# Performance work log

Hardware: AMD Instinct MI355X
Metric: run time of the kernel (lower is better)

## Reference

```python
import jax, jax.numpy as jnp
import numpy as np

K = 3          # B-spline order (cubic)
G = 10         # number of spline intervals over [0, 1]
NELY, NELX = 512, 512
WIDTHS = [2, 32, 32, 1]


def _make_grid(in_dim):
    # extended uniform knot vector over [0,1] with K extra knots each side: (in_dim, G+2K+1)
    h = 1.0 / G
    knots = jnp.arange(-K, G + K + 1, dtype=jnp.float32) * h
    return jnp.tile(knots[None, :], (in_dim, 1))


def setup_inputs() -> dict:
    key = jax.random.key(0)
    ks = jax.random.split(key, 1 + 3 * (len(WIDTHS) - 1))
    inp = {"coords": jax.random.uniform(ks[0], (NELY * NELX, 2), dtype=jnp.float32)}
    for l, (i, o) in enumerate(zip(WIDTHS[:-1], WIDTHS[1:])):
        inp[f"grid{l}"] = _make_grid(i)
        inp[f"coef{l}"] = 0.1 * jax.random.normal(ks[1 + 3 * l], (i, o, G + K), dtype=jnp.float32)
        inp[f"sb{l}"] = jax.random.normal(ks[2 + 3 * l], (i, o), dtype=jnp.float32) / np.sqrt(i).astype(np.float32)
        inp[f"sp{l}"] = jnp.ones((i, o), dtype=jnp.float32)
    inp["density_bias"] = jnp.full((1,), np.float32(np.log(0.5 / (1.0 - 0.5 + 1e-8))))
    return inp


def _b_batch(x, grid):
    # Cox-de Boor recursion. x: (B, in), grid: (in, G+2K+1) -> bases (B, in, G+K)
    xe = x[:, :, None]
    v = ((xe >= grid[None, :, :-1]) & (xe < grid[None, :, 1:])).astype(x.dtype)
    for p in range(1, K + 1):
        left = (xe - grid[None, :, : -(p + 1)]) / (grid[None, :, p:-1] - grid[None, :, : -(p + 1)])
        right = (grid[None, :, p + 1:] - xe) / (grid[None, :, p + 1:] - grid[None, :, 1:-p])
        v = left * v[:, :, :-1] + right * v[:, :, 1:]
    return v


def _kan_layer(x, grid, coef, sb, sp):
    # y_out = sum_in [ sb * silu(x) + sp * sum_k B_k(x) * coef_k ]
    B = _b_batch(x, grid)                               # (batch, in, G+K)
    spline = jnp.einsum('bik,iok->bio', B, coef)        # (batch, in, out)
    base = jax.nn.silu(x)                               # (batch, in)
    return jnp.sum(sb[None] * base[:, :, None] + sp[None] * spline, axis=1)


def reference(coords, grid0, coef0, sb0, sp0, grid1, coef1, sb1, sp1,
              grid2, coef2, sb2, sp2, density_bias):
    h = _kan_layer(coords, grid0, coef0, sb0, sp0)
    h = _kan_layer(h, grid1, coef1, sb1, sp1)
    logits = _kan_layer(h, grid2, coef2, sb2, sp2) + density_bias
    return jax.nn.sigmoid(logits).reshape(1, NELY, NELX)
```

## Files before the change

kernel.cpp:

```cpp
#include <hip/hip_runtime.h>
#include <hip/hip_bf16.h>

typedef __hip_bfloat16 bf16;
typedef __fp16 h2v __attribute__((ext_vector_type(2)));
typedef __fp16 half8 __attribute__((ext_vector_type(8)));
typedef float floatx4 __attribute__((ext_vector_type(4)));

#define NPTS (512*512)

#define OFF_BIAS 12
#define OFF_FLAG 13
#define OFF_BF   16
#define NFRAG    50
#define WS_WORDS (16 + NFRAG*64*4)


__device__ __forceinline__ bool sniff_f32(const void* g0) {
    float f = ((const float*)g0)[0];
    return fabsf(f + 0.3f) < 0.01f;
}
__device__ __forceinline__ float ld(const void* p, int i, bool f32) {
    return f32 ? ((const float*)p)[i] : __bfloat162float(((const bf16*)p)[i]);
}
__device__ __forceinline__ unsigned pk_rtn(float a, float b) {
    union { h2v v; unsigned u; } x;
    x.v[0] = (__fp16)a; x.v[1] = (__fp16)b;
    return x.u;
}
__device__ __forceinline__ unsigned pkf16(float a, float b) {
    union { h2v v; unsigned u; } x;
    x.v = __builtin_amdgcn_cvt_pkrtz(a, b);
    return x.u;
}

__device__ float slotval(int layer, int K, int o,
                         const void* c0, const void* sb0, const void* sp0,
                         const void* c1, const void* sb1, const void* sp1,
                         const void* c2, const void* sb2, const void* sp2, bool f32)
{
    int i = K >> 4, s = K & 15;
    if (layer == 2 && o != 0) return 0.0f;
    if (s >= 1 && s <= 13) {
        int m = s - 1;
        if (layer == 0) return ld(c0, (i*32+o)*13 + m, f32) * ld(sp0, i*32+o, f32);
        if (layer == 1) return ld(c1, (i*32+o)*13 + m, f32) * ld(sp1, i*32+o, f32);
        return ld(c2, i*13 + m, f32) * ld(sp2, i, f32);
    }
    if (s == 14) {
        if (layer == 0) return ld(sb0, i*32+o, f32);
        if (layer == 1) return ld(sb1, i*32+o, f32);
        return ld(sb2, i, f32);
    }
    return 0.0f;
}

__global__ __launch_bounds__(256) void kan_prep(
    const void* __restrict__ g0, const void* __restrict__ c0,
    const void* __restrict__ sb0, const void* __restrict__ sp0,
    const void* __restrict__ g1, const void* __restrict__ c1,
    const void* __restrict__ sb1, const void* __restrict__ sp1,
    const void* __restrict__ g2, const void* __restrict__ c2,
    const void* __restrict__ sb2, const void* __restrict__ sp2,
    const void* __restrict__ bias, float* __restrict__ ws)
{
    const bool f32 = sniff_f32(g0);
    int t = blockIdx.x * blockDim.x + threadIdx.x;

    if (t < 16) {
        if (t < 12) {
            int l = t >> 2, j = t & 3;
            const void* g = (l == 0) ? g0 : (l == 1) ? g1 : g2;
            float lo = ld(g, 0, f32), hi = ld(g, 16, f32);
            float ih = 16.0f / (hi - lo);
            float v = (j == 0) ? lo : (j == 1) ? hi
                    : (j == 2) ? ih : (-lo * ih);
            ws[t] = v;
        } else if (t == 12) ws[12] = ld(bias, 0, f32);
        else if (t == 13)   ws[13] = f32 ? 1.0f : 0.0f;
        else                ws[t] = 0.0f;
        return;
    }
    int ft = t - 16;
    if (ft >= NFRAG * 64) return;
    int f = ft >> 6, l = ft & 63, n = l & 15, q = l >> 4;
    int layer, c, nt;
    if (f < 2)       { layer = 0; c = 0;          nt = f; }
    else if (f < 34) { layer = 1; c = (f - 2) >> 1; nt = (f - 2) & 1; }
    else             { layer = 2; c = f - 34;     nt = 0; }
    int o = nt * 16 + n;
    unsigned wv[4];
#pragma unroll
    for (int jp = 0; jp < 4; jp++) {
        int K0 = c * 32 + q * 8 + jp * 2;
        float v0 = slotval(layer, K0,     o, c0,sb0,sp0, c1,sb1,sp1, c2,sb2,sp2, f32);
        float v1 = slotval(layer, K0 + 1, o, c0,sb0,sp0, c1,sb1,sp1, c2,sb2,sp2, f32);
        wv[jp] = pk_rtn(v0, v1);
    }
    uint4 out4; out4.x = wv[0]; out4.y = wv[1]; out4.z = wv[2]; out4.w = wv[3];
    ((uint4*)((unsigned*)ws + OFF_BF))[f * 64 + l] = out4;
}

__device__ __forceinline__ floatx4 mf(uint4 a, uint4 b, floatx4 c)
{
    union { uint4 u; half8 h; } ua, ub;
    ua.u = a; ub.u = b;
    return __builtin_amdgcn_mfma_f32_16x16x32_f16(ua.h, ub.h, c, 0, 0, 0);
}

__device__ __forceinline__ void eval_taps(float x, float ngh, float ih,
    unsigned& A, unsigned& B, unsigned& C, int& wout, float& si)
{
    float t  = fmaf(x, ih, ngh);
    float fj = floorf(t);
    float u  = t - fj;
    bool inb = (t >= 0.0f) && (t < 16.0f);
    float s6 = inb ? 0.166666667f : 0.0f;
    int j  = (int)fj;
    int jc = min(max(j, 0), 15);
    float u2 = u * u, u3 = u2 * u, om = 1.0f - u;
    float b0 = om * om * om * s6;
    float b1 = (fmaf(3.0f, u3, 4.0f) - 6.0f * u2) * s6;
    float b2 = fmaf(-3.0f, u3, fmaf(3.0f, u2, fmaf(3.0f, u, 1.0f))) * s6;
    float b3 = u3 * s6;
    int m0 = jc - 3;
    if ((unsigned)(m0 + 0) > 12u) b0 = 0.0f;
    if ((unsigned)(m0 + 1) > 12u) b1 = 0.0f;
    if ((unsigned)(m0 + 2) > 12u) b2 = 0.0f;
    if ((unsigned)(m0 + 3) > 12u) b3 = 0.0f;
    int s0 = m0 + 1;
    wout = ((s0 + 2) >> 1) - 1;
    if (s0 & 1) { A = pkf16(0.0f, b0); B = pkf16(b1, b2); C = pkf16(b3, 0.0f); }
    else        { A = pkf16(b0, b1);   B = pkf16(b2, b3); C = 0u; }
    si = x / (1.0f + __expf(-x));
}

__device__ __forceinline__ void stage2(unsigned* row, float f0, float f1,
                                       float ngh, float ih)
{
    uint4 z; z.x = 0u; z.y = 0u; z.z = 0u; z.w = 0u;
    *(uint4*)(row + 0)  = z;
    *(uint4*)(row + 4)  = z;
    *(uint4*)(row + 8)  = z;
    *(uint4*)(row + 12) = z;
    unsigned A0,B0,C0,A1,B1,C1; int w0,w1; float s0,s1;
    eval_taps(f0, ngh, ih, A0, B0, C0, w0, s0);
    eval_taps(f1, ngh, ih, A1, B1, C1, w1, s1);
    row[w0]     = A0; row[w0 + 1]  = B0; row[w0 + 2]  = C0;
    row[8 + w1] = A1; row[9 + w1]  = B1; row[10 + w1] = C1;
    row[7]  = pkf16(s0, 0.0f);
    row[15] = pkf16(s1, 0.0f);
}

__global__ __launch_bounds__(256, 4) void kan_main(
    const void* __restrict__ coords, const float* __restrict__ ws,
    void* __restrict__ out)
{
    __shared__ __align__(16) unsigned lds[4 * 2304];
    const unsigned* wsu = (const unsigned*)ws;
    const uint4* bfp = (const uint4*)(wsu + OFF_BF);

    int tid = threadIdx.x;
    int l = tid & 63, w = tid >> 6;
    int p = blockIdx.x * 256 + w * 64 + l;

    unsigned* rb = lds + w * 2304;
    unsigned* cb = rb;
    unsigned* myrow = cb + l * 20;

    const bool f32 = (ws[OFF_FLAG] != 0.0f);
    float x0, x1;
    if (f32) {
        float2 c = ((const float2*)coords)[p];
        x0 = c.x; x1 = c.y;
    } else {
        unsigned cc = ((const unsigned*)coords)[p];
        union { unsigned u; float f; } cv;
        cv.u = (cc & 0xffffu) << 16;  x0 = cv.f;
        cv.u = cc & 0xffff0000u;      x1 = cv.f;
    }

    const float iha = ws[2],  ngha = ws[3];
    const float ihb = ws[6],  nghb = ws[7];
    const float ihc = ws[10], nghc = ws[11];

    const int arow = l & 15, aq = (l >> 4) * 4;
    const int drow = (l >> 4) * 4, dcol = l & 15;

    float h[32];

    {
        floatx4 acc[4][2];
#pragma unroll
        for (int mt = 0; mt < 4; mt++)
#pragma unroll
            for (int nt = 0; nt < 2; nt++) acc[mt][nt] = (floatx4)0.0f;

        uint4 bf0 = bfp[0 * 64 + l], bf1 = bfp[1 * 64 + l];
        stage2(myrow, x0, x1, ngha, iha);
#pragma unroll
        for (int mt = 0; mt < 4; mt++) {
            uint4 a = *(const uint4*)(cb + (arow + 16 * mt) * 20 + aq);
            acc[mt][0] = mf(a, bf0, acc[mt][0]);
            acc[mt][1] = mf(a, bf1, acc[mt][1]);
        }
#pragma unroll
        for (int mt = 0; mt < 4; mt++)
#pragma unroll
            for (int nt = 0; nt < 2; nt++)
#pragma unroll
                for (int r = 0; r < 4; r++)
                    rb[(mt*16 + drow + r) * 36 + nt*16 + dcol] =
                        __float_as_uint(acc[mt][nt][r]);
#pragma unroll
        for (int q = 0; q < 8; q++) {
            uint4 v = *(const uint4*)(rb + l * 36 + q * 4);
            h[q*4+0] = __uint_as_float(v.x);
            h[q*4+1] = __uint_as_float(v.y);
            h[q*4+2] = __uint_as_float(v.z);
            h[q*4+3] = __uint_as_float(v.w);
        }
    }

    {
        floatx4 acc[4][2];
#pragma unroll
        for (int mt = 0; mt < 4; mt++)
#pragma unroll
            for (int nt = 0; nt < 2; nt++) acc[mt][nt] = (floatx4)0.0f;

#pragma unroll
        for (int c = 0; c < 16; c++) {
            uint4 bf0 = bfp[(2 + 2*c) * 64 + l];
            uint4 bf1 = bfp[(3 + 2*c) * 64 + l];
            stage2(myrow, h[2*c], h[2*c + 1], nghb, ihb);
#pragma unroll
            for (int mt = 0; mt < 4; mt++) {
                uint4 a = *(const uint4*)(cb + (arow + 16 * mt) * 20 + aq);
                acc[mt][0] = mf(a, bf0, acc[mt][0]);
                acc[mt][1] = mf(a, bf1, acc[mt][1]);
            }
        }
#pragma unroll
        for (int mt = 0; mt < 4; mt++)
#pragma unroll
            for (int nt = 0; nt < 2; nt++)
#pragma unroll
                for (int r = 0; r < 4; r++)
                    rb[(mt*16 + drow + r) * 36 + nt*16 + dcol] =
                        __float_as_uint(acc[mt][nt][r]);
#pragma unroll
        for (int q = 0; q < 8; q++) {
            uint4 v = *(const uint4*)(rb + l * 36 + q * 4);
            h[q*4+0] = __uint_as_float(v.x);
            h[q*4+1] = __uint_as_float(v.y);
            h[q*4+2] = __uint_as_float(v.z);
            h[q*4+3] = __uint_as_float(v.w);
        }
    }

    {
        floatx4 acc[4];
#pragma unroll
        for (int mt = 0; mt < 4; mt++) acc[mt] = (floatx4)0.0f;

#pragma unroll
        for (int c = 0; c < 16; c++) {
            uint4 bf = bfp[(34 + c) * 64 + l];
            stage2(myrow, h[2*c], h[2*c + 1], nghc, ihc);
#pragma unroll
            for (int mt = 0; mt < 4; mt++) {
                uint4 a = *(const uint4*)(cb + (arow + 16 * mt) * 20 + aq);
                acc[mt] = mf(a, bf, acc[mt]);
            }
        }
        if ((l & 15) == 0) {
#pragma unroll
            for (int mt = 0; mt < 4; mt++)
#pragma unroll
                for (int r = 0; r < 4; r++)
                    rb[(mt*16 + drow + r) * 36] = __float_as_uint(acc[mt][r]);
        }
        float z = __uint_as_float(rb[l * 36]);
        float r = 1.0f / (1.0f + __expf(-(z + ws[OFF_BIAS])));
        if (f32) ((float*)out)[p] = r;
        else     ((bf16*)out)[p] = __float2bfloat16(r);
    }
}

extern "C" void kernel_launch(void* const* d_in, const int* in_sizes, int n_in,
                              void* d_out, int out_size, void* d_ws, size_t ws_size,
                              hipStream_t stream)
{
    float* ws = (float*)d_ws;

    kan_prep<<<(16 + NFRAG*64 + 255) / 256, 256, 0, stream>>>(
        d_in[1], d_in[2], d_in[3], d_in[4],
        d_in[5], d_in[6], d_in[7], d_in[8],
        d_in[9], d_in[10], d_in[11], d_in[12],
        d_in[13], ws);

    kan_main<<<NPTS / 256, 256, 0, stream>>>(d_in[0], ws, d_out);
}
```

Measured before the change: 121.4 us.

## Double-buffer LDS spline staging and swizzle rows to avoid bank conflicts

The per-wave LDS staging area is split into two buffers so each chunk's A fragments are read before the next chunk's spline taps are written into the other buffer. This lets tap evaluation overlap with the MFMA work instead of serialising on a single row. Row offsets are swizzled by lane bits, with edge-case index redirection, to cut LDS bank conflicts. The hidden-state transpose now uses the two buffers, and blocks shrink to 128 threads. The swizzle edge handling adds complexity and some risk to correctness.

```diff
diff --git a/kernel.cpp b/kernel.cpp
--- a/kernel.cpp
+++ b/kernel.cpp
@@ -134,38 +134,44 @@
     si = x / (1.0f + __expf(-x));
 }
 
-__device__ __forceinline__ void stage2(unsigned* row, float f0, float f1,
+__device__ __forceinline__ void stage2(unsigned* row, int sw, float f0, float f1,
                                        float ngh, float ih)
 {
+    unsigned A0,B0,C0,A1,B1,C1; int w0,w1; float s0,s1;
+    eval_taps(f0, ngh, ih, A0, B0, C0, w0, s0);
+    eval_taps(f1, ngh, ih, A1, B1, C1, w1, s1);
     uint4 z; z.x = 0u; z.y = 0u; z.z = 0u; z.w = 0u;
     *(uint4*)(row + 0)  = z;
     *(uint4*)(row + 4)  = z;
     *(uint4*)(row + 8)  = z;
     *(uint4*)(row + 12) = z;
-    unsigned A0,B0,C0,A1,B1,C1; int w0,w1; float s0,s1;
-    eval_taps(f0, ngh, ih, A0, B0, C0, w0, s0);
-    eval_taps(f1, ngh, ih, A1, B1, C1, w1, s1);
-    row[w0]     = A0; row[w0 + 1]  = B0; row[w0 + 2]  = C0;
-    row[8 + w1] = A1; row[9 + w1]  = B1; row[10 + w1] = C1;
+    int wa = (w0 < 0) ? 0 : w0;
+    row[wa]     = A0; row[w0 + 1]  = B0; row[w0 + 2]  = C0;
+    int i2 = 10 + w1;
+    if (i2 > 15 && sw) i2 = -4;
+    row[8 + w1] = A1; row[9 + w1]  = B1; row[i2] = C1;
     row[7]  = pkf16(s0, 0.0f);
     row[15] = pkf16(s1, 0.0f);
 }
 
-__global__ __launch_bounds__(256, 4) void kan_main(
+__global__ __launch_bounds__(128, 4) void kan_main(
     const void* __restrict__ coords, const float* __restrict__ ws,
     void* __restrict__ out)
 {
-    __shared__ __align__(16) unsigned lds[4 * 2304];
+    __shared__ __align__(16) unsigned lds[2 * 2560];
     const unsigned* wsu = (const unsigned*)ws;
     const uint4* bfp = (const uint4*)(wsu + OFF_BF);
 
     int tid = threadIdx.x;
     int l = tid & 63, w = tid >> 6;
-    int p = blockIdx.x * 256 + w * 64 + l;
-
-    unsigned* rb = lds + w * 2304;
-    unsigned* cb = rb;
-    unsigned* myrow = cb + l * 20;
+    int p = blockIdx.x * 128 + w * 64 + l;
+
+    unsigned* buf0 = lds + w * 2560;
+    unsigned* buf1 = buf0 + 1280;
+    const int sw  = (l & 8)  ? 4 : 0;
+    const int swr = (l & 32) ? 4 : 0;
+    unsigned* row0 = buf0 + l * 20 + sw;
+    unsigned* row1 = buf1 + l * 20 + sw;
 
     const bool f32 = (ws[OFF_FLAG] != 0.0f);
     float x0, x1;
@@ -184,6 +190,7 @@
     const float ihc = ws[10], nghc = ws[11];
 
     const int arow = l & 15, aq = (l >> 4) * 4;
+    const int aoff = arow * 20 + sw + aq;
     const int drow = (l >> 4) * 4, dcol = l & 15;
 
     float h[32];
@@ -195,29 +202,30 @@
 #pragma unroll
             for (int nt = 0; nt < 2; nt++) acc[mt][nt] = (floatx4)0.0f;
 
+        stage2(row0, sw, x0, x1, ngha, iha);
         uint4 bf0 = bfp[0 * 64 + l], bf1 = bfp[1 * 64 + l];
-        stage2(myrow, x0, x1, ngha, iha);
 #pragma unroll
         for (int mt = 0; mt < 4; mt++) {
-            uint4 a = *(const uint4*)(cb + (arow + 16 * mt) * 20 + aq);
+            uint4 a = *(const uint4*)(buf0 + mt * 320 + aoff);
             acc[mt][0] = mf(a, bf0, acc[mt][0]);
             acc[mt][1] = mf(a, bf1, acc[mt][1]);
         }
 #pragma unroll
         for (int mt = 0; mt < 4; mt++)
 #pragma unroll
-            for (int nt = 0; nt < 2; nt++)
-#pragma unroll
-                for (int r = 0; r < 4; r++)
-                    rb[(mt*16 + drow + r) * 36 + nt*16 + dcol] =
-                        __float_as_uint(acc[mt][nt][r]);
-#pragma unroll
-        for (int q = 0; q < 8; q++) {
-            uint4 v = *(const uint4*)(rb + l * 36 + q * 4);
-            h[q*4+0] = __uint_as_float(v.x);
-            h[q*4+1] = __uint_as_float(v.y);
-            h[q*4+2] = __uint_as_float(v.z);
-            h[q*4+3] = __uint_as_float(v.w);
+            for (int r = 0; r < 4; r++) {
+                int rowi = (16*mt + drow + r) * 20 + swr + dcol;
+                buf0[rowi] = __float_as_uint(acc[mt][0][r]);
+                buf1[rowi] = __float_as_uint(acc[mt][1][r]);
+            }
+#pragma unroll
+        for (int q = 0; q < 4; q++) {
+            uint4 v0 = *(const uint4*)(buf0 + l * 20 + sw + 4 * q);
+            h[4*q+0]  = __uint_as_float(v0.x); h[4*q+1]  = __uint_as_float(v0.y);
+            h[4*q+2]  = __uint_as_float(v0.z); h[4*q+3]  = __uint_as_float(v0.w);
+            uint4 v1 = *(const uint4*)(buf1 + l * 20 + sw + 4 * q);
+            h[16+4*q+0] = __uint_as_float(v1.x); h[16+4*q+1] = __uint_as_float(v1.y);
+            h[16+4*q+2] = __uint_as_float(v1.z); h[16+4*q+3] = __uint_as_float(v1.w);
         }
     }
 
@@ -228,33 +236,40 @@
 #pragma unroll
             for (int nt = 0; nt < 2; nt++) acc[mt][nt] = (floatx4)0.0f;
 
+        stage2(row0, sw, h[0], h[1], nghb, ihb);
 #pragma unroll
         for (int c = 0; c < 16; c++) {
+            const unsigned* bc = (c & 1) ? buf1 : buf0;
+            unsigned* rn = (c & 1) ? row0 : row1;
+            uint4 a[4];
+#pragma unroll
+            for (int mt = 0; mt < 4; mt++)
+                a[mt] = *(const uint4*)(bc + mt * 320 + aoff);
+            if (c < 15) stage2(rn, sw, h[2*c+2], h[2*c+3], nghb, ihb);
             uint4 bf0 = bfp[(2 + 2*c) * 64 + l];
             uint4 bf1 = bfp[(3 + 2*c) * 64 + l];
-            stage2(myrow, h[2*c], h[2*c + 1], nghb, ihb);
 #pragma unroll
             for (int mt = 0; mt < 4; mt++) {
-                uint4 a = *(const uint4*)(cb + (arow + 16 * mt) * 20 + aq);
-                acc[mt][0] = mf(a, bf0, acc[mt][0]);
-                acc[mt][1] = mf(a, bf1, acc[mt][1]);
+                acc[mt][0] = mf(a[mt], bf0, acc[mt][0]);
+                acc[mt][1] = mf(a[mt], bf1, acc[mt][1]);
             }
         }
 #pragma unroll
         for (int mt = 0; mt < 4; mt++)
 #pragma unroll
-            for (int nt = 0; nt < 2; nt++)
-#pragma unroll
-                for (int r = 0; r < 4; r++)
-                    rb[(mt*16 + drow + r) * 36 + nt*16 + dcol] =
-                        __float_as_uint(acc[mt][nt][r]);
-#pragma unroll
-        for (int q = 0; q < 8; q++) {
-            uint4 v = *(const uint4*)(rb + l * 36 + q * 4);
-            h[q*4+0] = __uint_as_float(v.x);
-            h[q*4+1] = __uint_as_float(v.y);
-            h[q*4+2] = __uint_as_float(v.z);
-            h[q*4+3] = __uint_as_float(v.w);
+            for (int r = 0; r < 4; r++) {
+                int rowi = (16*mt + drow + r) * 20 + swr + dcol;
+                buf0[rowi] = __float_as_uint(acc[mt][0][r]);
+                buf1[rowi] = __float_as_uint(acc[mt][1][r]);
+            }
+#pragma unroll
+        for (int q = 0; q < 4; q++) {
+            uint4 v0 = *(const uint4*)(buf0 + l * 20 + sw + 4 * q);
+            h[4*q+0]  = __uint_as_float(v0.x); h[4*q+1]  = __uint_as_float(v0.y);
+            h[4*q+2]  = __uint_as_float(v0.z); h[4*q+3]  = __uint_as_float(v0.w);
+            uint4 v1 = *(const uint4*)(buf1 + l * 20 + sw + 4 * q);
+            h[16+4*q+0] = __uint_as_float(v1.x); h[16+4*q+1] = __uint_as_float(v1.y);
+            h[16+4*q+2] = __uint_as_float(v1.z); h[16+4*q+3] = __uint_as_float(v1.w);
         }
     }
 
@@ -263,24 +278,29 @@
 #pragma unroll
         for (int mt = 0; mt < 4; mt++) acc[mt] = (floatx4)0.0f;
 
+        stage2(row0, sw, h[0], h[1], nghc, ihc);
 #pragma unroll
         for (int c = 0; c < 16; c++) {
+            const unsigned* bc = (c & 1) ? buf1 : buf0;
+            unsigned* rn = (c & 1) ? row0 : row1;
+            uint4 a[4];
+#pragma unroll
+            for (int mt = 0; mt < 4; mt++)
+                a[mt] = *(const uint4*)(bc + mt * 320 + aoff);
+            if (c < 15) stage2(rn, sw, h[2*c+2], h[2*c+3], nghc, ihc);
             uint4 bf = bfp[(34 + c) * 64 + l];
-            stage2(myrow, h[2*c], h[2*c + 1], nghc, ihc);
-#pragma unroll
-            for (int mt = 0; mt < 4; mt++) {
-                uint4 a = *(const uint4*)(cb + (arow + 16 * mt) * 20 + aq);
-                acc[mt] = mf(a, bf, acc[mt]);
-            }
-        }
-        if ((l & 15) == 0) {
 #pragma unroll
             for (int mt = 0; mt < 4; mt++)
+                acc[mt] = mf(a[mt], bf, acc[mt]);
+        }
+        if (dcol == 0) {
+#pragma unroll
+            for (int mt = 0; mt < 4; mt++)
 #pragma unroll
                 for (int r = 0; r < 4; r++)
-                    rb[(mt*16 + drow + r) * 36] = __float_as_uint(acc[mt][r]);
-        }
-        float z = __uint_as_float(rb[l * 36]);
+                    buf0[(16*mt + drow + r) * 20 + swr] = __float_as_uint(acc[mt][r]);
+        }
+        float z = __uint_as_float(buf0[l * 20 + sw]);
         float r = 1.0f / (1.0f + __expf(-(z + ws[OFF_BIAS])));
         if (f32) ((float*)out)[p] = r;
         else     ((bf16*)out)[p] = __float2bfloat16(r);
@@ -299,5 +319,5 @@
         d_in[9], d_in[10], d_in[11], d_in[12],
         d_in[13], ws);
 
-    kan_main<<<NPTS / 256, 256, 0, stream>>>(d_in[0], ws, d_out);
-}
+    kan_main<<<NPTS / 128, 128, 0, stream>>>(d_in[0], ws, d_out);
+}
```

Result: slower. 124.5 us (+2.5%).
